# Kernel optimization log

Hardware: AMD Instinct MI355X
Metric: run time of the kernel (lower is better)

Reference implementation:

```python
import jax, jax.numpy as jnp
import numpy as np

B, S, D, H = 4, 2048, 1024, 16
HD = D // H  # head dim = 64


def setup_inputs() -> dict:
    key = jax.random.key(0)
    k1, k2, k3 = jax.random.split(key, 3)
    return {
        "hidden_states": jax.random.normal(k1, (B, S, D), dtype=jnp.float32),
        "w_attn": jax.random.normal(k2, (D, 3 * D), dtype=jnp.float32) * 0.02,
        "b_attn": jnp.zeros((3 * D,), dtype=jnp.float32),
        "w_proj": jax.random.normal(k3, (D, D), dtype=jnp.float32) * 0.02,
        "b_proj": jnp.zeros((D,), dtype=jnp.float32),
    }


def reference(hidden_states, w_attn, b_attn, w_proj, b_proj):
    b, s, d = hidden_states.shape
    # fused QKV projection (Conv1D == x @ W + b)
    qkv = hidden_states @ w_attn + b_attn  # [b, s, 3d]
    q, k, v = jnp.split(qkv, 3, axis=-1)

    def split_heads(x):  # [b, s, d] -> [b, h, s, hd]
        return x.reshape(b, s, H, HD).transpose(0, 2, 1, 3)

    q, k, v = split_heads(q), split_heads(k), split_heads(v)

    scores = jnp.einsum("bhqd,bhkd->bhqk", q, k)  # [b, h, s, s]
    causal = jnp.tril(jnp.ones((s, s), dtype=scores.dtype))
    # source masks before scaling: w*b + -1e5*(1-b), then / sqrt(head_dim)
    scores = scores * causal + (-100000.0) * (1.0 - causal)
    scores = scores / jnp.sqrt(jnp.asarray(HD, dtype=scores.dtype))

    attn = jax.nn.softmax(scores, axis=-1)  # attn dropout is identity (p=0)
    ctx = jnp.einsum("bhqk,bhkd->bhqd", attn, v)  # [b, h, s, hd]
    ctx = ctx.transpose(0, 2, 1, 3).reshape(b, s, d)  # merge heads
    out = ctx @ w_proj + b_proj  # resid dropout identity (p=0)
    return out
```

## Files before the change

### kernel.cpp

```cpp
#include <hip/hip_runtime.h>
#include <hip/hip_bf16.h>

#define BB 4
#define SS 2048
#define DD 1024
#define HH 16
#define HD 64
#define MM (BB * SS)
#define NQKV (3 * DD)

typedef __attribute__((ext_vector_type(8))) _Float16 half8;
typedef __attribute__((ext_vector_type(4))) float f32x4;

static __device__ __forceinline__ unsigned short f2h(float f) {
  _Float16 h = (_Float16)f;
  return __builtin_bit_cast(unsigned short, h);
}

static __device__ __forceinline__ void gload_lds16(const void* g, void* l) {
  __builtin_amdgcn_global_load_lds(
      (const __attribute__((address_space(1))) unsigned int*)g,
      (__attribute__((address_space(3))) unsigned int*)l, 16, 0, 0);
}

__global__ __launch_bounds__(256) void cvt_f16(const float* __restrict__ in,
                                               unsigned short* __restrict__ out,
                                               int n4) {
  int i = blockIdx.x * 256 + threadIdx.x;
  if (i < n4) {
    float4 v = ((const float4*)in)[i];
    ushort4 o;
    o.x = f2h(v.x); o.y = f2h(v.y); o.z = f2h(v.z); o.w = f2h(v.w);
    ((ushort4*)out)[i] = o;
  }
}

__global__ __launch_bounds__(256) void transpose_f16(
    const float* __restrict__ in, unsigned short* __restrict__ out, int K, int N) {
  __shared__ float tile[64][65];
  const int k0 = blockIdx.y * 64, n0 = blockIdx.x * 64;
  const int t = threadIdx.x;
#pragma unroll
  for (int i = 0; i < 16; ++i) {
    int idx = i * 256 + t;
    int r = idx >> 6, c = idx & 63;
    tile[r][c] = in[(size_t)(k0 + r) * N + n0 + c];
  }
  __syncthreads();
#pragma unroll
  for (int i = 0; i < 16; ++i) {
    int idx = i * 256 + t;
    int r = idx >> 6, c = idx & 63;
    out[(size_t)(n0 + r) * K + k0 + c] = f2h(tile[c][r]);
  }
}

template <int MODE>
__global__ __launch_bounds__(256) void gemm_f16(
    const unsigned short* __restrict__ A, const unsigned short* __restrict__ BT,
    const float* __restrict__ bias, unsigned short* __restrict__ Cq,
    unsigned short* __restrict__ vT, float* __restrict__ Cf, int M, int N, int K,
    int nx) {
  __shared__ __align__(16) unsigned short As[128 * 32];
  __shared__ __align__(16) unsigned short Bs[128 * 32];

  const int t = threadIdx.x;
  const int lane = t & 63;
  const int w = t >> 6;
  const int wr = w >> 1, wc = w & 1;

  const int nwg = gridDim.x;
  const int per = nwg >> 3;
  const int logical = (blockIdx.x & 7) * per + (blockIdx.x >> 3);
  const int bm = (logical / nx) * 128, bn = (logical % nx) * 128;

  f32x4 acc[4][4] = {};

  const int srow = (lane >> 2);
  const int sslot = (lane & 3);

  for (int k0 = 0; k0 < K; k0 += 32) {
    __syncthreads();
#pragma unroll
    for (int i = 0; i < 2; ++i) {
      int chunk = w * 2 + i;
      int row = chunk * 16 + srow;
      int cs = sslot ^ ((row >> 1) & 3);
      gload_lds16(A + (size_t)(bm + row) * K + k0 + cs * 8,
                  (char*)As + chunk * 1024);
      gload_lds16(BT + (size_t)(bn + row) * K + k0 + cs * 8,
                  (char*)Bs + chunk * 1024);
    }
    __syncthreads();

    half8 af[4], bf[4];
#pragma unroll
    for (int mb = 0; mb < 4; ++mb) {
      int row = wr * 64 + mb * 16 + (lane & 15);
      int cs = (lane >> 4) ^ ((row >> 1) & 3);
      af[mb] = *(const half8*)((const char*)As + row * 64 + cs * 16);
    }
#pragma unroll
    for (int nb = 0; nb < 4; ++nb) {
      int row = wc * 64 + nb * 16 + (lane & 15);
      int cs = (lane >> 4) ^ ((row >> 1) & 3);
      bf[nb] = *(const half8*)((const char*)Bs + row * 64 + cs * 16);
    }
    __builtin_amdgcn_s_setprio(1);
#pragma unroll
    for (int mb = 0; mb < 4; ++mb)
#pragma unroll
      for (int nb = 0; nb < 4; ++nb)
        acc[mb][nb] = __builtin_amdgcn_mfma_f32_16x16x32_f16(
            af[mb], bf[nb], acc[mb][nb], 0, 0, 0);
    __builtin_amdgcn_s_setprio(0);
  }

  const int g = lane >> 4;
#pragma unroll
  for (int mb = 0; mb < 4; ++mb) {
#pragma unroll
    for (int nb = 0; nb < 4; ++nb) {
      int m0 = bm + wr * 64 + mb * 16 + g * 4;
      int n = bn + wc * 64 + nb * 16 + (lane & 15);
      float bv = bias[n];
      if (MODE == 0) {
        if (n < 2 * DD) {
#pragma unroll
          for (int r = 0; r < 4; ++r)
            Cq[(size_t)(m0 + r) * NQKV + n] = f2h(acc[mb][nb][r] + bv);
        } else {
          int h = (n - 2 * DD) >> 6;
          int hd = n & 63;
          int b = m0 >> 11, s0 = m0 & 2047;
          ushort4 pk;
          unsigned short* pp = (unsigned short*)&pk;
#pragma unroll
          for (int r = 0; r < 4; ++r) pp[r] = f2h(acc[mb][nb][r] + bv);
          *(ushort4*)&vT[((size_t)((b * HH + h) * HD + hd)) * SS + s0] = pk;
        }
      } else {
#pragma unroll
        for (int r = 0; r < 4; ++r)
          Cf[(size_t)(m0 + r) * N + n] = acc[mb][nb][r] + bv;
      }
    }
  }
}

__global__ __launch_bounds__(256, 4) void flash16(
    const unsigned short* __restrict__ qkv,
    const unsigned short* __restrict__ vT,
    unsigned short* __restrict__ ctx) {
  __shared__ __align__(16) unsigned short Kt[2][64 * 64];
  __shared__ __align__(16) unsigned short Vt[2][64 * 64];
  __shared__ __align__(16) unsigned short Ps[4][16 * 64];

  const int tid = threadIdx.x, lane = tid & 63, w = tid >> 6;
  const int phys = blockIdx.x;
  const int logical = (phys & 7) * 128 + (phys >> 3);
  const int bh = logical >> 4;
  const int p = logical & 15;
  const int b = bh >> 4, h = bh & 15;
  const int qHiB = 31 - p;

  const int q = lane & 15, g = lane >> 4;
  const int qrowLo = p * 64 + w * 16 + q;
  const int qrowHi = qHiB * 64 + w * 16 + q;

  const unsigned short* kg = qkv + (size_t)b * SS * NQKV + DD + h * HD;
  const unsigned short* vg = vT + (size_t)(b * HH + h) * HD * SS;

  half8 qfLo[2], qfHi[2];
  {
    const unsigned short* qp = qkv + (size_t)(b * SS + qrowLo) * NQKV + h * HD;
    qfLo[0] = *(const half8*)(qp + g * 8);
    qfLo[1] = *(const half8*)(qp + 32 + g * 8);
    const unsigned short* qp2 = qkv + (size_t)(b * SS + qrowHi) * NQKV + h * HD;
    qfHi[0] = *(const half8*)(qp2 + g * 8);
    qfHi[1] = *(const half8*)(qp2 + 32 + g * 8);
  }

  f32x4 oLo[4] = {}, oHi[4] = {};
  float mLo = -1e30f, lLo = 0.f, mHi = -1e30f, lHi = 0.f;

  unsigned short* pw = &Ps[w][0];
  const int srow = lane >> 3, sslot = lane & 7;

  auto STAGE = [&](int tt, int c) {
    const int k0s = tt * 64;
#pragma unroll
    for (int i = 0; i < 2; ++i) {
      int chunk = w * 2 + i;
      int row = chunk * 8 + srow;
      int cs = sslot ^ (row & 7);
      gload_lds16(kg + (size_t)(k0s + row) * NQKV + cs * 8,
                  (char*)Kt[c] + chunk * 1024);
      gload_lds16(vg + (size_t)row * SS + k0s + cs * 8,
                  (char*)Vt[c] + chunk * 1024);
    }
  };

  auto QBLOCK = [&](const half8 (&qf)[2], f32x4 (&oa)[4], float& m_run,
                    float& l_run, int qrow, int k0, int cur, bool diag) {
    f32x4 sa[4] = {};
    __builtin_amdgcn_s_setprio(1);
#pragma unroll
    for (int ks = 0; ks < 2; ++ks)
#pragma unroll
      for (int kb = 0; kb < 4; ++kb) {
        int row = kb * 16 + q;
        int cs = (g + 4 * ks) ^ (row & 7);
        half8 kf = *(const half8*)((const char*)Kt[cur] + row * 128 + cs * 16);
        sa[kb] =
            __builtin_amdgcn_mfma_f32_16x16x32_f16(kf, qf[ks], sa[kb], 0, 0, 0);
      }
    __builtin_amdgcn_s_setprio(0);

    float pmax = -1e30f;
#pragma unroll
    for (int kb = 0; kb < 4; ++kb)
#pragma unroll
      for (int r = 0; r < 4; ++r) {
        float v = sa[kb][r] * 0.125f;
        if (diag) {
          int kk = k0 + kb * 16 + g * 4 + r;
          if (kk > qrow) v = -12500.f;
        }
        sa[kb][r] = v;
        pmax = fmaxf(pmax, v);
      }
    pmax = fmaxf(pmax, __shfl_xor(pmax, 16));
    pmax = fmaxf(pmax, __shfl_xor(pmax, 32));
    if (!__all(pmax - m_run <= 8.0f)) {
      float mnew = fmaxf(m_run, pmax);
      float sc = __expf(m_run - mnew);
      l_run *= sc;
#pragma unroll
      for (int hb = 0; hb < 4; ++hb) oa[hb] *= sc;
      m_run = mnew;
    }
    float lsum = 0.f;
#pragma unroll
    for (int kb = 0; kb < 4; ++kb) {
      ushort4 pk;
      unsigned short* pp = (unsigned short*)&pk;
#pragma unroll
      for (int r = 0; r < 4; ++r) {
        float pv = __expf(sa[kb][r] - m_run);
        lsum += pv;
        pp[r] = f2h(pv);
      }
      int slot = (2 * kb + (g >> 1)) ^ (q & 7);
      *(ushort4*)((char*)pw + q * 128 + slot * 16 + (g & 1) * 8) = pk;
    }
    lsum += __shfl_xor(lsum, 16);
    lsum += __shfl_xor(lsum, 32);
    l_run += lsum;

    __builtin_amdgcn_s_setprio(1);
#pragma unroll
    for (int ks = 0; ks < 2; ++ks) {
      int pslot = (g + 4 * ks) ^ (q & 7);
      half8 pf = *(const half8*)((const char*)pw + q * 128 + pslot * 16);
#pragma unroll
      for (int hb = 0; hb < 4; ++hb) {
        int row = hb * 16 + q;
        int cs = (g + 4 * ks) ^ (row & 7);
        half8 vf = *(const half8*)((const char*)Vt[cur] + row * 128 + cs * 16);
        oa[hb] =
            __builtin_amdgcn_mfma_f32_16x16x32_f16(vf, pf, oa[hb], 0, 0, 0);
      }
    }
    __builtin_amdgcn_s_setprio(0);
  };

  STAGE(0, 0);
  __syncthreads();

  const int nt = qHiB + 1;
  for (int t = 0; t < nt; ++t) {
    const int cur = t & 1;
    if (t + 1 < nt) STAGE(t + 1, cur ^ 1);
    const int k0 = t * 64;
    if (t <= p) QBLOCK(qfLo, oLo, mLo, lLo, qrowLo, k0, cur, t == p);
    QBLOCK(qfHi, oHi, mHi, lHi, qrowHi, k0, cur, t == qHiB);
    __syncthreads();
  }

  {
    float inv = 1.f / lLo;
    unsigned short* cp = ctx + (size_t)(b * SS + qrowLo) * DD + h * HD;
#pragma unroll
    for (int hb = 0; hb < 4; ++hb) {
      ushort4 pk;
      unsigned short* pp = (unsigned short*)&pk;
#pragma unroll
      for (int r = 0; r < 4; ++r) pp[r] = f2h(oLo[hb][r] * inv);
      *(ushort4*)(cp + hb * 16 + g * 4) = pk;
    }
  }
  {
    float inv = 1.f / lHi;
    unsigned short* cp = ctx + (size_t)(b * SS + qrowHi) * DD + h * HD;
#pragma unroll
    for (int hb = 0; hb < 4; ++hb) {
      ushort4 pk;
      unsigned short* pp = (unsigned short*)&pk;
#pragma unroll
      for (int r = 0; r < 4; ++r) pp[r] = f2h(oHi[hb][r] * inv);
      *(ushort4*)(cp + hb * 16 + g * 4) = pk;
    }
  }
}

extern "C" void kernel_launch(void* const* d_in, const int* in_sizes, int n_in,
                              void* d_out, int out_size, void* d_ws,
                              size_t ws_size, hipStream_t stream) {
  const float* x = (const float*)d_in[0];
  const float* w_attn = (const float*)d_in[1];
  const float* b_attn = (const float*)d_in[2];
  const float* w_proj = (const float*)d_in[3];
  const float* b_proj = (const float*)d_in[4];
  float* out = (float*)d_out;

  unsigned short* xB = (unsigned short*)d_ws;
  unsigned short* qkvB = xB + (size_t)MM * DD;
  unsigned short* vTb = qkvB + (size_t)MM * NQKV;
  unsigned short* ctxB = vTb + (size_t)BB * HH * HD * SS;
  unsigned short* wqkvT = ctxB + (size_t)MM * DD;
  unsigned short* wprojT = wqkvT + (size_t)NQKV * DD;

  cvt_f16<<<dim3(MM * DD / 4 / 256), 256, 0, stream>>>(x, xB, MM * DD / 4);
  transpose_f16<<<dim3(NQKV / 64, DD / 64), 256, 0, stream>>>(w_attn, wqkvT, DD,
                                                              NQKV);
  transpose_f16<<<dim3(DD / 64, DD / 64), 256, 0, stream>>>(w_proj, wprojT, DD,
                                                            DD);

  gemm_f16<0><<<dim3((NQKV / 128) * (MM / 128)), 256, 0, stream>>>(
      xB, wqkvT, b_attn, qkvB, vTb, nullptr, MM, NQKV, DD, NQKV / 128);

  flash16<<<dim3(1024), 256, 0, stream>>>(qkvB, vTb, ctxB);

  gemm_f16<1><<<dim3((DD / 128) * (MM / 128)), 256, 0, stream>>>(
      ctxB, wprojT, b_proj, nullptr, nullptr, out, MM, DD, DD, DD / 128);
}
```

Measured before the change: 295.3 us.

## Double-buffer GEMM LDS staging and use exp2 with prescaled scores in flash

The GEMM kernel now uses two LDS buffers, issuing the next K-slice's global-to-LDS loads before computing on the current one. This removes one barrier per iteration and overlaps loads with MFMA, at the cost of doubled LDS and a launch bound of four blocks per CU. Separately, the flash attention kernel folds log2(e) into the score scale, so it can call the hardware exp2 instead of __expf. The mask constant and rescale threshold are adjusted to match the base-2 domain.

```diff
diff --git a/kernel.cpp b/kernel.cpp
--- a/kernel.cpp
+++ b/kernel.cpp
@@ -56,13 +56,13 @@
 }
 
 template <int MODE>
-__global__ __launch_bounds__(256) void gemm_f16(
+__global__ __launch_bounds__(256, 4) void gemm_f16(
     const unsigned short* __restrict__ A, const unsigned short* __restrict__ BT,
     const float* __restrict__ bias, unsigned short* __restrict__ Cq,
     unsigned short* __restrict__ vT, float* __restrict__ Cf, int M, int N, int K,
     int nx) {
-  __shared__ __align__(16) unsigned short As[128 * 32];
-  __shared__ __align__(16) unsigned short Bs[128 * 32];
+  __shared__ __align__(16) unsigned short As[2][128 * 32];
+  __shared__ __align__(16) unsigned short Bs[2][128 * 32];
 
   const int t = threadIdx.x;
   const int lane = t & 63;
@@ -79,32 +79,39 @@
   const int srow = (lane >> 2);
   const int sslot = (lane & 3);
 
-  for (int k0 = 0; k0 < K; k0 += 32) {
-    __syncthreads();
+  auto STAGE = [&](int k0, int c) {
 #pragma unroll
     for (int i = 0; i < 2; ++i) {
       int chunk = w * 2 + i;
       int row = chunk * 16 + srow;
       int cs = sslot ^ ((row >> 1) & 3);
       gload_lds16(A + (size_t)(bm + row) * K + k0 + cs * 8,
-                  (char*)As + chunk * 1024);
+                  (char*)As[c] + chunk * 1024);
       gload_lds16(BT + (size_t)(bn + row) * K + k0 + cs * 8,
-                  (char*)Bs + chunk * 1024);
-    }
-    __syncthreads();
+                  (char*)Bs[c] + chunk * 1024);
+    }
+  };
+
+  STAGE(0, 0);
+  __syncthreads();
+
+  const int nsteps = K >> 5;
+  for (int ks = 0; ks < nsteps; ++ks) {
+    const int cur = ks & 1;
+    if (ks + 1 < nsteps) STAGE((ks + 1) * 32, cur ^ 1);
 
     half8 af[4], bf[4];
 #pragma unroll
     for (int mb = 0; mb < 4; ++mb) {
       int row = wr * 64 + mb * 16 + (lane & 15);
       int cs = (lane >> 4) ^ ((row >> 1) & 3);
-      af[mb] = *(const half8*)((const char*)As + row * 64 + cs * 16);
+      af[mb] = *(const half8*)((const char*)As[cur] + row * 64 + cs * 16);
     }
 #pragma unroll
     for (int nb = 0; nb < 4; ++nb) {
       int row = wc * 64 + nb * 16 + (lane & 15);
       int cs = (lane >> 4) ^ ((row >> 1) & 3);
-      bf[nb] = *(const half8*)((const char*)Bs + row * 64 + cs * 16);
+      bf[nb] = *(const half8*)((const char*)Bs[cur] + row * 64 + cs * 16);
     }
     __builtin_amdgcn_s_setprio(1);
 #pragma unroll
@@ -114,6 +121,7 @@
         acc[mb][nb] = __builtin_amdgcn_mfma_f32_16x16x32_f16(
             af[mb], bf[nb], acc[mb][nb], 0, 0, 0);
     __builtin_amdgcn_s_setprio(0);
+    __syncthreads();
   }
 
   const int g = lane >> 4;
@@ -148,6 +156,9 @@
   }
 }
 
+#define C2F 0.180336880f
+#define MASK2 -18000.0f
+
 __global__ __launch_bounds__(256, 4) void flash16(
     const unsigned short* __restrict__ qkv,
     const unsigned short* __restrict__ vT,
@@ -222,19 +233,19 @@
     for (int kb = 0; kb < 4; ++kb)
 #pragma unroll
       for (int r = 0; r < 4; ++r) {
-        float v = sa[kb][r] * 0.125f;
+        float v = sa[kb][r] * C2F;
         if (diag) {
           int kk = k0 + kb * 16 + g * 4 + r;
-          if (kk > qrow) v = -12500.f;
+          if (kk > qrow) v = MASK2;
         }
         sa[kb][r] = v;
         pmax = fmaxf(pmax, v);
       }
     pmax = fmaxf(pmax, __shfl_xor(pmax, 16));
     pmax = fmaxf(pmax, __shfl_xor(pmax, 32));
-    if (!__all(pmax - m_run <= 8.0f)) {
+    if (!__all(pmax - m_run <= 11.5f)) {
       float mnew = fmaxf(m_run, pmax);
-      float sc = __expf(m_run - mnew);
+      float sc = __builtin_amdgcn_exp2f(m_run - mnew);
       l_run *= sc;
 #pragma unroll
       for (int hb = 0; hb < 4; ++hb) oa[hb] *= sc;
@@ -247,7 +258,7 @@
       unsigned short* pp = (unsigned short*)&pk;
 #pragma unroll
       for (int r = 0; r < 4; ++r) {
-        float pv = __expf(sa[kb][r] - m_run);
+        float pv = __builtin_amdgcn_exp2f(sa[kb][r] - m_run);
         lsum += pv;
         pp[r] = f2h(pv);
       }
```

Measured after the change: 288.7 us. 1.02x faster.
